# Performance work log

Measured on AMD Instinct MI355X. Metric: run time of the kernel, lower is better.

The kernel has to match this reference:

```python
import jax, jax.numpy as jnp
import numpy as np

I, H = 4, 64


def setup_inputs() -> dict:
    key = jax.random.key(0)
    ks = jax.random.split(key, 7)
    s_ih = 1.0 / np.sqrt(H)
    return {
        "x": jax.random.normal(ks[0], (8192, 512, I), dtype=jnp.float32),
        "W_ih": jax.random.uniform(ks[1], (4 * H, I), minval=-s_ih, maxval=s_ih, dtype=jnp.float32),
        "W_hh": jax.random.uniform(ks[2], (4 * H, H), minval=-s_ih, maxval=s_ih, dtype=jnp.float32),
        "b_ih": jax.random.uniform(ks[3], (4 * H,), minval=-s_ih, maxval=s_ih, dtype=jnp.float32),
        "b_hh": jax.random.uniform(ks[4], (4 * H,), minval=-s_ih, maxval=s_ih, dtype=jnp.float32),
        "W_fc": jax.random.uniform(ks[5], (1, H), minval=-s_ih, maxval=s_ih, dtype=jnp.float32),
        "b_fc": jax.random.uniform(ks[6], (1,), minval=-s_ih, maxval=s_ih, dtype=jnp.float32),
    }


def _lstm_last_hidden(x, W_ih, W_hh, b_ih, b_hh):
    # x: [B, T, I] batch_first; PyTorch gate order: i, f, g, o
    B = x.shape[0]
    # Precompute input projections for all timesteps in one GEMM: [T, B, 4H]
    xg = jnp.einsum('bti,gi->tbg', x, W_ih) + (b_ih + b_hh)

    def step(carry, xg_t):
        h, c = carry
        gates = xg_t + h @ W_hh.T  # [B, 4H]
        i, f, g, o = jnp.split(gates, 4, axis=-1)
        i = jax.nn.sigmoid(i)
        f = jax.nn.sigmoid(f)
        g = jnp.tanh(g)
        o = jax.nn.sigmoid(o)
        c = f * c + i * g
        h = o * jnp.tanh(c)
        return (h, c), None

    h0 = jnp.zeros((B, W_hh.shape[1]), dtype=x.dtype)
    c0 = jnp.zeros_like(h0)
    (h_n, _), _ = jax.lax.scan(step, (h0, c0), xg)
    return h_n  # [B, H]


def reference(x, W_ih, W_hh, b_ih, b_hh, W_fc, b_fc):
    h_n = _lstm_last_hidden(x, W_ih, W_hh, b_ih, b_hh)
    return h_n @ W_fc.T + b_fc  # [B, 1]
```

## Files before the change

### kernel.cpp

```cpp
#include <hip/hip_runtime.h>


typedef float f32x4 __attribute__((ext_vector_type(4)));
typedef _Float16 f16x8 __attribute__((ext_vector_type(8)));
typedef _Float16 f16x4 __attribute__((ext_vector_type(4)));

#define TSEQ 512
#define IDIM 4
#define BPB 16
#define TCH 32
#define L2E 1.44269504088896340736f

#if __has_builtin(__builtin_amdgcn_exp2f)
#define EX2(v) __builtin_amdgcn_exp2f(v)
#else
#define EX2(v) exp2f(v)
#endif
#define RCP(v) __builtin_amdgcn_rcpf(v)

__global__ __launch_bounds__(256, 2) void lstm_fused(
    const float* __restrict__ x,
    const float* __restrict__ W_ih,
    const float* __restrict__ W_hh,
    const float* __restrict__ b_ih,
    const float* __restrict__ b_hh,
    const float* __restrict__ W_fc,
    const float* __restrict__ b_fc,
    float* __restrict__ out)
{
    __shared__ __align__(16) _Float16 hbuf[2][BPB * 64];
    __shared__ __align__(8)  f16x4    xstage[BPB * 33];

    const int tid  = threadIdx.x;
    const int lane = tid & 63;
    const int wv   = tid >> 6;
    const int b0   = blockIdx.x * BPB;
    const int r    = lane & 15;
    const int g16  = lane >> 4;

    f16x8 bfrag[4][3];
    float bias[4];
    #pragma unroll
    for (int t4 = 0; t4 < 4; ++t4) {
        const float sc = (t4 == 2) ? 2.0f * L2E : L2E;
        const int g = t4 * 64 + wv * 16 + r;
        #pragma unroll
        for (int ks = 0; ks < 2; ++ks) {
            const float* p = W_hh + g * 64 + ks * 32 + g16 * 8;
            f16x8 f;
            #pragma unroll
            for (int j = 0; j < 8; ++j) f[j] = (_Float16)(p[j] * sc);
            bfrag[t4][ks] = f;
        }
        f16x8 f;
        #pragma unroll
        for (int j = 0; j < 8; ++j) f[j] = (_Float16)0.0f;
        if (g16 == 0) {
            #pragma unroll
            for (int j = 0; j < 4; ++j) f[j] = (_Float16)(W_ih[g * IDIM + j] * sc);
        }
        bfrag[t4][2] = f;
        bias[t4] = (b_ih[g] + b_hh[g]) * sc;
    }
    const float wfc = W_fc[lane];
    const float bfc = b_fc[0];

    float c_reg[4] = {0.f, 0.f, 0.f, 0.f};
    for (int i = tid; i < BPB * 64; i += 256) hbuf[0][i] = (_Float16)0.0f;

    const int bb0 = tid >> 5, tf = tid & 31;
    const float* xg0 = x + ((size_t)(b0 + bb0)     * TSEQ + tf) * IDIM;
    const float* xg1 = x + ((size_t)(b0 + bb0 + 8) * TSEQ + tf) * IDIM;
    float4 xn0 = *(const float4*)xg0;
    float4 xn1 = *(const float4*)xg1;

    const int hbase = r * 128;
    const int hs0 = ((g16 + 0) << 4) ^ ((r & 7) << 4);
    const int hs1 = ((g16 + 4) << 4) ^ ((r & 7) << 4);
    int hw[4];
    #pragma unroll
    for (int q = 0; q < 4; ++q) {
        const int bat = 4 * g16 + q;
        hw[q] = (bat * 128 + (wv * 16 + r) * 2) ^ ((bat & 7) << 4);
    }
    char* hb0 = (char*)&hbuf[0][0];
    char* hb1 = (char*)&hbuf[1][0];

    auto step = [&](int tt, const char* rb, char* wb) {
        f16x8 a0 = *(const f16x8*)(rb + hbase + hs0);
        f16x8 a1 = *(const f16x8*)(rb + hbase + hs1);
        f16x4 xv = f16x4{(_Float16)0.f, (_Float16)0.f, (_Float16)0.f, (_Float16)0.f};
        if (g16 == 0) xv = xstage[r * 33 + tt];
        f16x8 ax;
        ax[0] = xv[0]; ax[1] = xv[1]; ax[2] = xv[2]; ax[3] = xv[3];
        ax[4] = (_Float16)0.f; ax[5] = (_Float16)0.f;
        ax[6] = (_Float16)0.f; ax[7] = (_Float16)0.f;

        f32x4 acc[4];
        __builtin_amdgcn_s_setprio(1);
        #pragma unroll
        for (int t4 = 0; t4 < 4; ++t4) {
            f32x4 a; a[0] = a[1] = a[2] = a[3] = bias[t4];
            a = __builtin_amdgcn_mfma_f32_16x16x32_f16(a0, bfrag[t4][0], a, 0, 0, 0);
            a = __builtin_amdgcn_mfma_f32_16x16x32_f16(a1, bfrag[t4][1], a, 0, 0, 0);
            a = __builtin_amdgcn_mfma_f32_16x16x32_f16(ax, bfrag[t4][2], a, 0, 0, 0);
            acc[t4] = a;
        }
        __builtin_amdgcn_s_setprio(0);

        #pragma unroll
        for (int q = 0; q < 4; ++q) {
            float ei = EX2(-acc[0][q]);
            float ef = EX2(-acc[1][q]);
            float eg = EX2(-acc[2][q]);
            float eo = EX2(-acc[3][q]);
            float ig = (1.f - eg) * RCP((1.f + ei) * (1.f + eg));
            float ff = RCP(1.f + ef);
            float c  = ff * c_reg[q] + ig;
            c_reg[q] = c;
            float uc = fminf(fmaxf(c * (2.0f * L2E), -60.f), 60.f);
            float et = EX2(-uc);
            float h  = (1.f - et) * RCP((1.f + eo) * (1.f + et));
            *(_Float16*)(wb + hw[q]) = (_Float16)h;
        }
        __syncthreads();
    };

    for (int tc = 0; tc < TSEQ; tc += TCH) {
        f16x4 s0, s1;
        s0[0] = (_Float16)xn0.x; s0[1] = (_Float16)xn0.y;
        s0[2] = (_Float16)xn0.z; s0[3] = (_Float16)xn0.w;
        s1[0] = (_Float16)xn1.x; s1[1] = (_Float16)xn1.y;
        s1[2] = (_Float16)xn1.z; s1[3] = (_Float16)xn1.w;
        xstage[bb0 * 33 + tf]       = s0;
        xstage[(bb0 + 8) * 33 + tf] = s1;
        __syncthreads();
        if (tc + TCH < TSEQ) {
            xn0 = *(const float4*)(xg0 + (tc + TCH) * IDIM);
            xn1 = *(const float4*)(xg1 + (tc + TCH) * IDIM);
        }
        for (int tt = 0; tt < TCH; tt += 2) {
            step(tt,     hb0, hb1);
            step(tt + 1, hb1, hb0);
        }
    }

    #pragma unroll
    for (int q = 0; q < 4; ++q) {
        const int bat = 4 * wv + q;
        const int byte = (bat * 128 + lane * 2) ^ ((bat & 7) << 4);
        float hv = (float)*(const _Float16*)(hb0 + byte);
        float partial = hv * wfc;
        #pragma unroll
        for (int off = 32; off > 0; off >>= 1)
            partial += __shfl_down(partial, off);
        if (lane == 0) out[b0 + bat] = partial + bfc;
    }
}

extern "C" void kernel_launch(void* const* d_in, const int* in_sizes, int n_in,
                              void* d_out, int out_size, void* d_ws, size_t ws_size,
                              hipStream_t stream) {
    const float* x    = (const float*)d_in[0];
    const float* W_ih = (const float*)d_in[1];
    const float* W_hh = (const float*)d_in[2];
    const float* b_ih = (const float*)d_in[3];
    const float* b_hh = (const float*)d_in[4];
    const float* W_fc = (const float*)d_in[5];
    const float* b_fc = (const float*)d_in[6];
    float* out = (float*)d_out;

    const int B = in_sizes[0] / (TSEQ * IDIM);
    lstm_fused<<<B / BPB, 256, 0, stream>>>(x, W_ih, W_hh, b_ih, b_hh, W_fc, b_fc, out);
}
```

Measured before the change: 330.2 us.

## Halve batch per block and split gate nonlinearities across wave halves

Each block now handles 8 batch rows instead of 16, with launch bounds raised to 4 blocks per CU so more independent recurrences are resident. The MFMA tile is still 16 rows wide, so half of its rows are zero padding; lanes exchange accumulator halves via xor-32 shuffles so every lane computes transcendentals for only 2 useful rows instead of 4. The bias is folded into the x-projection MFMA as a hi/lo fp16 pair multiplied by constant ones, which frees the bias registers. The cost is half-wasted MFMA work, extra shuffles, and a small precision change in the bias.

```diff
diff --git a/kernel.cpp b/kernel.cpp
--- a/kernel.cpp
+++ b/kernel.cpp
@@ -7,7 +7,7 @@
 
 #define TSEQ 512
 #define IDIM 4
-#define BPB 16
+#define BPB 8
 #define TCH 32
 #define L2E 1.44269504088896340736f
 
@@ -18,7 +18,7 @@
 #endif
 #define RCP(v) __builtin_amdgcn_rcpf(v)
 
-__global__ __launch_bounds__(256, 2) void lstm_fused(
+__global__ __launch_bounds__(256, 4) void lstm_fused(
     const float* __restrict__ x,
     const float* __restrict__ W_ih,
     const float* __restrict__ W_hh,
@@ -28,8 +28,8 @@
     const float* __restrict__ b_fc,
     float* __restrict__ out)
 {
-    __shared__ __align__(16) _Float16 hbuf[2][BPB * 64];
-    __shared__ __align__(8)  f16x4    xstage[BPB * 33];
+    __shared__ __align__(16) _Float16 hbuf[2][16 * 64];
+    __shared__ __align__(8)  f16x4    xstage[16 * 33];
 
     const int tid  = threadIdx.x;
     const int lane = tid & 63;
@@ -39,7 +39,6 @@
     const int g16  = lane >> 4;
 
     f16x8 bfrag[4][3];
-    float bias[4];
     #pragma unroll
     for (int t4 = 0; t4 < 4; ++t4) {
         const float sc = (t4 == 2) ? 2.0f * L2E : L2E;
@@ -58,62 +57,78 @@
         if (g16 == 0) {
             #pragma unroll
             for (int j = 0; j < 4; ++j) f[j] = (_Float16)(W_ih[g * IDIM + j] * sc);
+            float biasf = (b_ih[g] + b_hh[g]) * sc;
+            _Float16 hi = (_Float16)biasf;
+            f[4] = hi;
+            f[5] = (_Float16)(biasf - (float)hi);
         }
         bfrag[t4][2] = f;
-        bias[t4] = (b_ih[g] + b_hh[g]) * sc;
     }
     const float wfc = W_fc[lane];
     const float bfc = b_fc[0];
+    const f32x4 zero4 = {0.f, 0.f, 0.f, 0.f};
 
-    float c_reg[4] = {0.f, 0.f, 0.f, 0.f};
-    for (int i = tid; i < BPB * 64; i += 256) hbuf[0][i] = (_Float16)0.0f;
+    float c_reg[2] = {0.f, 0.f};
+    for (int i = tid; i < 2 * 16 * 64; i += 256) ((_Float16*)hbuf)[i] = (_Float16)0.0f;
+    {
+        f16x4 z; z[0] = z[1] = z[2] = z[3] = (_Float16)0.0f;
+        for (int i = tid; i < 16 * 33; i += 256) xstage[i] = z;
+    }
 
-    const int bb0 = tid >> 5, tf = tid & 31;
-    const float* xg0 = x + ((size_t)(b0 + bb0)     * TSEQ + tf) * IDIM;
-    const float* xg1 = x + ((size_t)(b0 + bb0 + 8) * TSEQ + tf) * IDIM;
-    float4 xn0 = *(const float4*)xg0;
-    float4 xn1 = *(const float4*)xg1;
+    const int bb = tid >> 5, tf = tid & 31;
+    const float* xg = x + ((size_t)(b0 + bb) * TSEQ + tf) * IDIM;
+    float4 xn = *(const float4*)xg;
 
     const int hbase = r * 128;
     const int hs0 = ((g16 + 0) << 4) ^ ((r & 7) << 4);
     const int hs1 = ((g16 + 4) << 4) ^ ((r & 7) << 4);
-    int hw[4];
+    const int bat0 = ((g16 & 1) << 2) | ((g16 >> 1) << 1);
+    int hwb[2];
     #pragma unroll
-    for (int q = 0; q < 4; ++q) {
-        const int bat = 4 * g16 + q;
-        hw[q] = (bat * 128 + (wv * 16 + r) * 2) ^ ((bat & 7) << 4);
+    for (int q = 0; q < 2; ++q) {
+        const int bat = bat0 + q;
+        hwb[q] = (bat * 128 + (wv * 16 + r) * 2) ^ ((bat & 7) << 4);
     }
+    const bool lowhalf = (lane < 32);
     char* hb0 = (char*)&hbuf[0][0];
     char* hb1 = (char*)&hbuf[1][0];
 
     auto step = [&](int tt, const char* rb, char* wb) {
         f16x8 a0 = *(const f16x8*)(rb + hbase + hs0);
         f16x8 a1 = *(const f16x8*)(rb + hbase + hs1);
-        f16x4 xv = f16x4{(_Float16)0.f, (_Float16)0.f, (_Float16)0.f, (_Float16)0.f};
-        if (g16 == 0) xv = xstage[r * 33 + tt];
+        f16x4 xv = xstage[r * 33 + tt];
         f16x8 ax;
         ax[0] = xv[0]; ax[1] = xv[1]; ax[2] = xv[2]; ax[3] = xv[3];
-        ax[4] = (_Float16)0.f; ax[5] = (_Float16)0.f;
-        ax[6] = (_Float16)0.f; ax[7] = (_Float16)0.f;
+        ax[4] = (_Float16)1.0f; ax[5] = (_Float16)1.0f;
+        ax[6] = (_Float16)0.0f; ax[7] = (_Float16)0.0f;
 
         f32x4 acc[4];
         __builtin_amdgcn_s_setprio(1);
         #pragma unroll
         for (int t4 = 0; t4 < 4; ++t4) {
-            f32x4 a; a[0] = a[1] = a[2] = a[3] = bias[t4];
-            a = __builtin_amdgcn_mfma_f32_16x16x32_f16(a0, bfrag[t4][0], a, 0, 0, 0);
+            f32x4 a;
+            a = __builtin_amdgcn_mfma_f32_16x16x32_f16(a0, bfrag[t4][0], zero4, 0, 0, 0);
             a = __builtin_amdgcn_mfma_f32_16x16x32_f16(a1, bfrag[t4][1], a, 0, 0, 0);
             a = __builtin_amdgcn_mfma_f32_16x16x32_f16(ax, bfrag[t4][2], a, 0, 0, 0);
             acc[t4] = a;
         }
         __builtin_amdgcn_s_setprio(0);
 
+        float v[4][2];
         #pragma unroll
-        for (int q = 0; q < 4; ++q) {
-            float ei = EX2(-acc[0][q]);
-            float ef = EX2(-acc[1][q]);
-            float eg = EX2(-acc[2][q]);
-            float eo = EX2(-acc[3][q]);
+        for (int t4 = 0; t4 < 4; ++t4) {
+            float u2 = __shfl_xor(acc[t4][2], 32);
+            float u3 = __shfl_xor(acc[t4][3], 32);
+            v[t4][0] = lowhalf ? acc[t4][0] : u2;
+            v[t4][1] = lowhalf ? acc[t4][1] : u3;
+        }
+
+        #pragma unroll
+        for (int q = 0; q < 2; ++q) {
+            float ei = EX2(-v[0][q]);
+            float ef = EX2(-v[1][q]);
+            float eg = EX2(-v[2][q]);
+            float eo = EX2(-v[3][q]);
             float ig = (1.f - eg) * RCP((1.f + ei) * (1.f + eg));
             float ff = RCP(1.f + ef);
             float c  = ff * c_reg[q] + ig;
@@ -121,24 +136,20 @@
             float uc = fminf(fmaxf(c * (2.0f * L2E), -60.f), 60.f);
             float et = EX2(-uc);
             float h  = (1.f - et) * RCP((1.f + eo) * (1.f + et));
-            *(_Float16*)(wb + hw[q]) = (_Float16)h;
+            *(_Float16*)(wb + hwb[q]) = (_Float16)h;
         }
         __syncthreads();
     };
 
     for (int tc = 0; tc < TSEQ; tc += TCH) {
-        f16x4 s0, s1;
-        s0[0] = (_Float16)xn0.x; s0[1] = (_Float16)xn0.y;
-        s0[2] = (_Float16)xn0.z; s0[3] = (_Float16)xn0.w;
-        s1[0] = (_Float16)xn1.x; s1[1] = (_Float16)xn1.y;
-        s1[2] = (_Float16)xn1.z; s1[3] = (_Float16)xn1.w;
-        xstage[bb0 * 33 + tf]       = s0;
-        xstage[(bb0 + 8) * 33 + tf] = s1;
+        f16x4 s;
+        s[0] = (_Float16)xn.x; s[1] = (_Float16)xn.y;
+        s[2] = (_Float16)xn.z; s[3] = (_Float16)xn.w;
+        xstage[bb * 33 + tf] = s;
         __syncthreads();
-        if (tc + TCH < TSEQ) {
-            xn0 = *(const float4*)(xg0 + (tc + TCH) * IDIM);
-            xn1 = *(const float4*)(xg1 + (tc + TCH) * IDIM);
-        }
+        if (tc + TCH < TSEQ) xn = *(const float4*)(xg + (tc + TCH) * IDIM);
+
+        #pragma unroll 2
         for (int tt = 0; tt < TCH; tt += 2) {
             step(tt,     hb0, hb1);
             step(tt + 1, hb1, hb0);
@@ -146,8 +157,8 @@
     }
 
     #pragma unroll
-    for (int q = 0; q < 4; ++q) {
-        const int bat = 4 * wv + q;
+    for (int q = 0; q < 2; ++q) {
+        const int bat = wv * 2 + q;
         const int byte = (bat * 128 + lane * 2) ^ ((bat & 7) << 4);
         float hv = (float)*(const _Float16*)(hb0 + byte);
         float partial = hv * wfc;
```

New measurement: 450.2 us. 1.36x slower.

## Process two interleaved 16-row batch groups per block and fold bias into MFMA

Applied to the files above, without the earlier changes.

Each block now handles 32 batch rows as two independent 16-row groups, issuing both groups' MFMAs before either group's gate nonlinearities. This lets one group's matrix work overlap the other's transcendental math and halves the barriers per row. The bias moves into the input-projection MFMA as an fp16 hi/lo pair multiplied by constant ones, which frees the accumulator-initialisation registers. In exchange the grid is halved and launch bounds drop to one block per SIMD group, so occupancy falls and register pressure rises.

```diff
diff --git a/kernel.cpp b/kernel.cpp
--- a/kernel.cpp
+++ b/kernel.cpp
@@ -7,7 +7,7 @@
 
 #define TSEQ 512
 #define IDIM 4
-#define BPB 16
+#define BPB 32
 #define TCH 32
 #define L2E 1.44269504088896340736f
 
@@ -18,7 +18,7 @@
 #endif
 #define RCP(v) __builtin_amdgcn_rcpf(v)
 
-__global__ __launch_bounds__(256, 2) void lstm_fused(
+__global__ __launch_bounds__(256, 1) void lstm_fused(
     const float* __restrict__ x,
     const float* __restrict__ W_ih,
     const float* __restrict__ W_hh,
@@ -28,8 +28,8 @@
     const float* __restrict__ b_fc,
     float* __restrict__ out)
 {
-    __shared__ __align__(16) _Float16 hbuf[2][BPB * 64];
-    __shared__ __align__(8)  f16x4    xstage[BPB * 33];
+    __shared__ __align__(16) _Float16 hbuf[2][2][16 * 64];
+    __shared__ __align__(8)  f16x4    xstage[2][16][33];
 
     const int tid  = threadIdx.x;
     const int lane = tid & 63;
@@ -39,7 +39,6 @@
     const int g16  = lane >> 4;
 
     f16x8 bfrag[4][3];
-    float bias[4];
     #pragma unroll
     for (int t4 = 0; t4 < 4; ++t4) {
         const float sc = (t4 == 2) ? 2.0f * L2E : L2E;
@@ -58,21 +57,29 @@
         if (g16 == 0) {
             #pragma unroll
             for (int j = 0; j < 4; ++j) f[j] = (_Float16)(W_ih[g * IDIM + j] * sc);
+            float biasf = (b_ih[g] + b_hh[g]) * sc;
+            _Float16 hi = (_Float16)biasf;
+            f[4] = hi;
+            f[5] = (_Float16)(biasf - (float)hi);
         }
         bfrag[t4][2] = f;
-        bias[t4] = (b_ih[g] + b_hh[g]) * sc;
     }
     const float wfc = W_fc[lane];
     const float bfc = b_fc[0];
-
-    float c_reg[4] = {0.f, 0.f, 0.f, 0.f};
-    for (int i = tid; i < BPB * 64; i += 256) hbuf[0][i] = (_Float16)0.0f;
-
-    const int bb0 = tid >> 5, tf = tid & 31;
-    const float* xg0 = x + ((size_t)(b0 + bb0)     * TSEQ + tf) * IDIM;
-    const float* xg1 = x + ((size_t)(b0 + bb0 + 8) * TSEQ + tf) * IDIM;
-    float4 xn0 = *(const float4*)xg0;
-    float4 xn1 = *(const float4*)xg1;
+    const f32x4 zero4 = {0.f, 0.f, 0.f, 0.f};
+
+    float c0[4] = {0.f, 0.f, 0.f, 0.f};
+    float c1[4] = {0.f, 0.f, 0.f, 0.f};
+    for (int i = tid; i < 2 * 16 * 64; i += 256)
+        ((_Float16*)&hbuf[0][0][0])[i] = (_Float16)0.0f;
+
+    const int row  = tid >> 3;
+    const int grp  = row >> 4, lrow = row & 15;
+    const int st0  = (tid & 7) * 4;
+    const float* xg = x + ((size_t)(b0 + row) * TSEQ + st0) * IDIM;
+    float4 xp[4];
+    #pragma unroll
+    for (int j = 0; j < 4; ++j) xp[j] = *(const float4*)(xg + j * IDIM);
 
     const int hbase = r * 128;
     const int hs0 = ((g16 + 0) << 4) ^ ((r & 7) << 4);
@@ -83,31 +90,13 @@
         const int bat = 4 * g16 + q;
         hw[q] = (bat * 128 + (wv * 16 + r) * 2) ^ ((bat & 7) << 4);
     }
-    char* hb0 = (char*)&hbuf[0][0];
-    char* hb1 = (char*)&hbuf[1][0];
-
-    auto step = [&](int tt, const char* rb, char* wb) {
-        f16x8 a0 = *(const f16x8*)(rb + hbase + hs0);
-        f16x8 a1 = *(const f16x8*)(rb + hbase + hs1);
-        f16x4 xv = f16x4{(_Float16)0.f, (_Float16)0.f, (_Float16)0.f, (_Float16)0.f};
-        if (g16 == 0) xv = xstage[r * 33 + tt];
-        f16x8 ax;
-        ax[0] = xv[0]; ax[1] = xv[1]; ax[2] = xv[2]; ax[3] = xv[3];
-        ax[4] = (_Float16)0.f; ax[5] = (_Float16)0.f;
-        ax[6] = (_Float16)0.f; ax[7] = (_Float16)0.f;
-
-        f32x4 acc[4];
-        __builtin_amdgcn_s_setprio(1);
-        #pragma unroll
-        for (int t4 = 0; t4 < 4; ++t4) {
-            f32x4 a; a[0] = a[1] = a[2] = a[3] = bias[t4];
-            a = __builtin_amdgcn_mfma_f32_16x16x32_f16(a0, bfrag[t4][0], a, 0, 0, 0);
-            a = __builtin_amdgcn_mfma_f32_16x16x32_f16(a1, bfrag[t4][1], a, 0, 0, 0);
-            a = __builtin_amdgcn_mfma_f32_16x16x32_f16(ax, bfrag[t4][2], a, 0, 0, 0);
-            acc[t4] = a;
-        }
-        __builtin_amdgcn_s_setprio(0);
-
+    char* hb[2][2];
+    #pragma unroll
+    for (int p = 0; p < 2; ++p)
+        #pragma unroll
+        for (int g = 0; g < 2; ++g) hb[p][g] = (char*)&hbuf[p][g][0];
+
+    auto upd = [&](const f32x4* acc, float* cr, char* wb) {
         #pragma unroll
         for (int q = 0; q < 4; ++q) {
             float ei = EX2(-acc[0][q]);
@@ -116,45 +105,87 @@
             float eo = EX2(-acc[3][q]);
             float ig = (1.f - eg) * RCP((1.f + ei) * (1.f + eg));
             float ff = RCP(1.f + ef);
-            float c  = ff * c_reg[q] + ig;
-            c_reg[q] = c;
+            float c  = ff * cr[q] + ig;
+            cr[q] = c;
             float uc = fminf(fmaxf(c * (2.0f * L2E), -60.f), 60.f);
             float et = EX2(-uc);
             float h  = (1.f - et) * RCP((1.f + eo) * (1.f + et));
             *(_Float16*)(wb + hw[q]) = (_Float16)h;
         }
+    };
+
+    auto mfma12 = [&](f16x8 a0, f16x8 a1, f16x8 ax, f32x4* acc) {
+        __builtin_amdgcn_s_setprio(1);
+        #pragma unroll
+        for (int t4 = 0; t4 < 4; ++t4) {
+            f32x4 a;
+            a = __builtin_amdgcn_mfma_f32_16x16x32_f16(a0, bfrag[t4][0], zero4, 0, 0, 0);
+            a = __builtin_amdgcn_mfma_f32_16x16x32_f16(a1, bfrag[t4][1], a, 0, 0, 0);
+            a = __builtin_amdgcn_mfma_f32_16x16x32_f16(ax, bfrag[t4][2], a, 0, 0, 0);
+            acc[t4] = a;
+        }
+        __builtin_amdgcn_s_setprio(0);
+    };
+
+    auto step = [&](int tt, const char* rb0, const char* rb1, char* wb0, char* wb1) {
+        f16x8 a00 = *(const f16x8*)(rb0 + hbase + hs0);
+        f16x8 a01 = *(const f16x8*)(rb0 + hbase + hs1);
+        f16x4 xv0 = xstage[0][r][tt];
+        f16x8 ax0;
+        ax0[0] = xv0[0]; ax0[1] = xv0[1]; ax0[2] = xv0[2]; ax0[3] = xv0[3];
+        ax0[4] = (_Float16)1.0f; ax0[5] = (_Float16)1.0f;
+        ax0[6] = (_Float16)0.0f; ax0[7] = (_Float16)0.0f;
+        f32x4 acc0[4];
+        mfma12(a00, a01, ax0, acc0);
+
+        f16x8 a10 = *(const f16x8*)(rb1 + hbase + hs0);
+        f16x8 a11 = *(const f16x8*)(rb1 + hbase + hs1);
+        f16x4 xv1 = xstage[1][r][tt];
+        f16x8 ax1;
+        ax1[0] = xv1[0]; ax1[1] = xv1[1]; ax1[2] = xv1[2]; ax1[3] = xv1[3];
+        ax1[4] = (_Float16)1.0f; ax1[5] = (_Float16)1.0f;
+        ax1[6] = (_Float16)0.0f; ax1[7] = (_Float16)0.0f;
+        f32x4 acc1[4];
+        mfma12(a10, a11, ax1, acc1);
+
+        upd(acc0, c0, wb0);
+        upd(acc1, c1, wb1);
         __syncthreads();
     };
 
     for (int tc = 0; tc < TSEQ; tc += TCH) {
-        f16x4 s0, s1;
-        s0[0] = (_Float16)xn0.x; s0[1] = (_Float16)xn0.y;
-        s0[2] = (_Float16)xn0.z; s0[3] = (_Float16)xn0.w;
-        s1[0] = (_Float16)xn1.x; s1[1] = (_Float16)xn1.y;
-        s1[2] = (_Float16)xn1.z; s1[3] = (_Float16)xn1.w;
-        xstage[bb0 * 33 + tf]       = s0;
-        xstage[(bb0 + 8) * 33 + tf] = s1;
+        #pragma unroll
+        for (int j = 0; j < 4; ++j) {
+            f16x4 s;
+            s[0] = (_Float16)xp[j].x; s[1] = (_Float16)xp[j].y;
+            s[2] = (_Float16)xp[j].z; s[3] = (_Float16)xp[j].w;
+            xstage[grp][lrow][st0 + j] = s;
+        }
         __syncthreads();
         if (tc + TCH < TSEQ) {
-            xn0 = *(const float4*)(xg0 + (tc + TCH) * IDIM);
-            xn1 = *(const float4*)(xg1 + (tc + TCH) * IDIM);
+            #pragma unroll
+            for (int j = 0; j < 4; ++j)
+                xp[j] = *(const float4*)(xg + ((tc + TCH) + j) * IDIM);
         }
         for (int tt = 0; tt < TCH; tt += 2) {
-            step(tt,     hb0, hb1);
-            step(tt + 1, hb1, hb0);
-        }
-    }
-
-    #pragma unroll
-    for (int q = 0; q < 4; ++q) {
-        const int bat = 4 * wv + q;
-        const int byte = (bat * 128 + lane * 2) ^ ((bat & 7) << 4);
-        float hv = (float)*(const _Float16*)(hb0 + byte);
-        float partial = hv * wfc;
-        #pragma unroll
-        for (int off = 32; off > 0; off >>= 1)
-            partial += __shfl_down(partial, off);
-        if (lane == 0) out[b0 + bat] = partial + bfc;
+            step(tt,     hb[0][0], hb[0][1], hb[1][0], hb[1][1]);
+            step(tt + 1, hb[1][0], hb[1][1], hb[0][0], hb[0][1]);
+        }
+    }
+
+    #pragma unroll
+    for (int g = 0; g < 2; ++g) {
+        #pragma unroll
+        for (int q = 0; q < 4; ++q) {
+            const int bat = wv * 4 + q;
+            const int byte = (bat * 128 + lane * 2) ^ ((bat & 7) << 4);
+            float hv = (float)*(const _Float16*)(hb[0][g] + byte);
+            float partial = hv * wfc;
+            #pragma unroll
+            for (int off = 32; off > 0; off >>= 1)
+                partial += __shfl_down(partial, off);
+            if (lane == 0) out[b0 + g * 16 + bat] = partial + bfc;
+        }
     }
 }
 
```

New measurement: 412.1 us. 1.25x slower.

## Ping-pong two batch groups per block to overlap MFMA with gate transcendentals

Applied to the files above, without the earlier changes.

Each block now handles 32 sequences as two 16-row groups of four waves each. The groups alternate phases, so one group's MFMA gate matmul runs while the other group's sigmoid/tanh activation math runs, with a barrier between phases. This aims to hide the serial MFMA-then-transcendental latency of each recurrent step. It also folds the bias into the input MFMA using hi/lo fp16 bias columns, and simplifies the cell update to need one fewer reciprocal. The cost is twice as many barriers per timestep and larger 512-thread blocks, which may lower occupancy.

```diff
diff --git a/kernel.cpp b/kernel.cpp
--- a/kernel.cpp
+++ b/kernel.cpp
@@ -7,7 +7,7 @@
 
 #define TSEQ 512
 #define IDIM 4
-#define BPB 16
+#define BPB 32
 #define TCH 32
 #define L2E 1.44269504088896340736f
 
@@ -18,7 +18,7 @@
 #endif
 #define RCP(v) __builtin_amdgcn_rcpf(v)
 
-__global__ __launch_bounds__(256, 2) void lstm_fused(
+__global__ __launch_bounds__(512, 2) void lstm_fused(
     const float* __restrict__ x,
     const float* __restrict__ W_ih,
     const float* __restrict__ W_hh,
@@ -28,22 +28,23 @@
     const float* __restrict__ b_fc,
     float* __restrict__ out)
 {
-    __shared__ __align__(16) _Float16 hbuf[2][BPB * 64];
-    __shared__ __align__(8)  f16x4    xstage[BPB * 33];
+    __shared__ __align__(16) _Float16 hbuf[2][2][16 * 64];
+    __shared__ __align__(8)  f16x4    xstage[2][16][33];
 
     const int tid  = threadIdx.x;
     const int lane = tid & 63;
     const int wv   = tid >> 6;
+    const int grp  = wv >> 2;
+    const int wvl  = wv & 3;
     const int b0   = blockIdx.x * BPB;
     const int r    = lane & 15;
     const int g16  = lane >> 4;
 
     f16x8 bfrag[4][3];
-    float bias[4];
     #pragma unroll
     for (int t4 = 0; t4 < 4; ++t4) {
         const float sc = (t4 == 2) ? 2.0f * L2E : L2E;
-        const int g = t4 * 64 + wv * 16 + r;
+        const int g = t4 * 64 + wvl * 16 + r;
         #pragma unroll
         for (int ks = 0; ks < 2; ++ks) {
             const float* p = W_hh + g * 64 + ks * 32 + g16 * 8;
@@ -58,21 +59,27 @@
         if (g16 == 0) {
             #pragma unroll
             for (int j = 0; j < 4; ++j) f[j] = (_Float16)(W_ih[g * IDIM + j] * sc);
+            float biasf = (b_ih[g] + b_hh[g]) * sc;
+            _Float16 hi = (_Float16)biasf;
+            f[4] = hi;
+            f[5] = (_Float16)(biasf - (float)hi);
         }
         bfrag[t4][2] = f;
-        bias[t4] = (b_ih[g] + b_hh[g]) * sc;
     }
     const float wfc = W_fc[lane];
     const float bfc = b_fc[0];
+    const f32x4 zero4 = {0.f, 0.f, 0.f, 0.f};
 
     float c_reg[4] = {0.f, 0.f, 0.f, 0.f};
-    for (int i = tid; i < BPB * 64; i += 256) hbuf[0][i] = (_Float16)0.0f;
-
-    const int bb0 = tid >> 5, tf = tid & 31;
-    const float* xg0 = x + ((size_t)(b0 + bb0)     * TSEQ + tf) * IDIM;
-    const float* xg1 = x + ((size_t)(b0 + bb0 + 8) * TSEQ + tf) * IDIM;
-    float4 xn0 = *(const float4*)xg0;
-    float4 xn1 = *(const float4*)xg1;
+    for (int i = tid; i < 2 * 16 * 64; i += 512)
+        ((_Float16*)&hbuf[0][0][0])[i] = (_Float16)0.0f;
+
+    const int xrow = tid >> 4;
+    const int xgp  = xrow >> 4, xlr = xrow & 15;
+    const int xtf  = tid & 15;
+    const float* xg = x + ((size_t)(b0 + xrow) * TSEQ + 2 * xtf) * IDIM;
+    float4 xn0 = *(const float4*)xg;
+    float4 xn1 = *(const float4*)(xg + IDIM);
 
     const int hbase = r * 128;
     const int hs0 = ((g16 + 0) << 4) ^ ((r & 7) << 4);
@@ -81,80 +88,107 @@
     #pragma unroll
     for (int q = 0; q < 4; ++q) {
         const int bat = 4 * g16 + q;
-        hw[q] = (bat * 128 + (wv * 16 + r) * 2) ^ ((bat & 7) << 4);
-    }
-    char* hb0 = (char*)&hbuf[0][0];
-    char* hb1 = (char*)&hbuf[1][0];
-
-    auto step = [&](int tt, const char* rb, char* wb) {
+        hw[q] = (bat * 128 + (wvl * 16 + r) * 2) ^ ((bat & 7) << 4);
+    }
+    char* hbB = (char*)&hbuf[0][0][0];
+    const int gofs = grp * 2048;
+    const f16x4* xsb = &xstage[grp][r][0];
+
+    auto STAGE = [&]() {
+        f16x4 s0, s1;
+        s0[0] = (_Float16)xn0.x; s0[1] = (_Float16)xn0.y;
+        s0[2] = (_Float16)xn0.z; s0[3] = (_Float16)xn0.w;
+        s1[0] = (_Float16)xn1.x; s1[1] = (_Float16)xn1.y;
+        s1[2] = (_Float16)xn1.z; s1[3] = (_Float16)xn1.w;
+        xstage[xgp][xlr][2 * xtf]     = s0;
+        xstage[xgp][xlr][2 * xtf + 1] = s1;
+    };
+
+    auto MFMA = [&](int parity, int tt, f32x4* acc) {
+        const char* rb = hbB + parity * 4096 + gofs;
         f16x8 a0 = *(const f16x8*)(rb + hbase + hs0);
         f16x8 a1 = *(const f16x8*)(rb + hbase + hs1);
-        f16x4 xv = f16x4{(_Float16)0.f, (_Float16)0.f, (_Float16)0.f, (_Float16)0.f};
-        if (g16 == 0) xv = xstage[r * 33 + tt];
+        f16x4 xv = xsb[tt];
         f16x8 ax;
         ax[0] = xv[0]; ax[1] = xv[1]; ax[2] = xv[2]; ax[3] = xv[3];
-        ax[4] = (_Float16)0.f; ax[5] = (_Float16)0.f;
-        ax[6] = (_Float16)0.f; ax[7] = (_Float16)0.f;
-
-        f32x4 acc[4];
+        ax[4] = (_Float16)1.0f; ax[5] = (_Float16)1.0f;
+        ax[6] = (_Float16)0.0f; ax[7] = (_Float16)0.0f;
         __builtin_amdgcn_s_setprio(1);
         #pragma unroll
         for (int t4 = 0; t4 < 4; ++t4) {
-            f32x4 a; a[0] = a[1] = a[2] = a[3] = bias[t4];
-            a = __builtin_amdgcn_mfma_f32_16x16x32_f16(a0, bfrag[t4][0], a, 0, 0, 0);
+            f32x4 a;
+            a = __builtin_amdgcn_mfma_f32_16x16x32_f16(a0, bfrag[t4][0], zero4, 0, 0, 0);
             a = __builtin_amdgcn_mfma_f32_16x16x32_f16(a1, bfrag[t4][1], a, 0, 0, 0);
             a = __builtin_amdgcn_mfma_f32_16x16x32_f16(ax, bfrag[t4][2], a, 0, 0, 0);
             acc[t4] = a;
         }
         __builtin_amdgcn_s_setprio(0);
-
+    };
+
+    auto TRANS = [&](int parityW, const f32x4* acc) {
+        char* wb = hbB + parityW * 4096 + gofs;
         #pragma unroll
         for (int q = 0; q < 4; ++q) {
             float ei = EX2(-acc[0][q]);
             float ef = EX2(-acc[1][q]);
             float eg = EX2(-acc[2][q]);
             float eo = EX2(-acc[3][q]);
-            float ig = (1.f - eg) * RCP((1.f + ei) * (1.f + eg));
-            float ff = RCP(1.f + ef);
-            float c  = ff * c_reg[q] + ig;
+            float A  = 1.f + ei, F = 1.f + ef;
+            float Gp = 1.f + eg, Gm = 1.f - eg;
+            float P   = A * Gp;
+            float num = c_reg[q] * P + Gm * F;
+            float c   = num * RCP(P * F);
             c_reg[q] = c;
             float uc = fminf(fmaxf(c * (2.0f * L2E), -60.f), 60.f);
             float et = EX2(-uc);
             float h  = (1.f - et) * RCP((1.f + eo) * (1.f + et));
             *(_Float16*)(wb + hw[q]) = (_Float16)h;
         }
+    };
+
+    STAGE();
+    __syncthreads();
+    xn0 = *(const float4*)(xg + TCH * IDIM);
+    xn1 = *(const float4*)(xg + TCH * IDIM + IDIM);
+
+    f32x4 acc[4];
+    if (grp == 0) MFMA(0, 0, acc);
+    __syncthreads();
+    if (grp == 0) TRANS(1, acc);
+    else          MFMA(0, 0, acc);
+    __syncthreads();
+
+    for (int t = 1; t < TSEQ; ++t) {
+        if ((t & (TCH - 1)) == 0) {
+            STAGE();
+            __syncthreads();
+            if (t + TCH < TSEQ) {
+                xn0 = *(const float4*)(xg + (size_t)(t + TCH) * IDIM);
+                xn1 = *(const float4*)(xg + (size_t)(t + TCH) * IDIM + IDIM);
+            }
+        }
+        const int tt = t & (TCH - 1);
+        const int p  = t & 1;
+        if (grp == 0) MFMA(p, tt, acc);
+        else          TRANS(p, acc);
         __syncthreads();
-    };
-
-    for (int tc = 0; tc < TSEQ; tc += TCH) {
-        f16x4 s0, s1;
-        s0[0] = (_Float16)xn0.x; s0[1] = (_Float16)xn0.y;
-        s0[2] = (_Float16)xn0.z; s0[3] = (_Float16)xn0.w;
-        s1[0] = (_Float16)xn1.x; s1[1] = (_Float16)xn1.y;
-        s1[2] = (_Float16)xn1.z; s1[3] = (_Float16)xn1.w;
-        xstage[bb0 * 33 + tf]       = s0;
-        xstage[(bb0 + 8) * 33 + tf] = s1;
+        if (grp == 0) TRANS(p ^ 1, acc);
+        else          MFMA(p, tt, acc);
         __syncthreads();
-        if (tc + TCH < TSEQ) {
-            xn0 = *(const float4*)(xg0 + (tc + TCH) * IDIM);
-            xn1 = *(const float4*)(xg1 + (tc + TCH) * IDIM);
-        }
-        for (int tt = 0; tt < TCH; tt += 2) {
-            step(tt,     hb0, hb1);
-            step(tt + 1, hb1, hb0);
-        }
-    }
+    }
+    if (grp == 1) TRANS(0, acc);
+    __syncthreads();
 
     #pragma unroll
     for (int q = 0; q < 4; ++q) {
-        const int bat = 4 * wv + q;
+        const int bat  = wvl * 4 + q;
         const int byte = (bat * 128 + lane * 2) ^ ((bat & 7) << 4);
-        float hv = (float)*(const _Float16*)(hb0 + byte);
+        float hv = (float)*(const _Float16*)(hbB + gofs + byte);
         float partial = hv * wfc;
         #pragma unroll
         for (int off = 32; off > 0; off >>= 1)
             partial += __shfl_down(partial, off);
-        if (lane == 0) out[b0 + bat] = partial + bfc;
+        if (lane == 0) out[b0 + grp * 16 + bat] = partial + bfc;
     }
 }
 
@@ -171,5 +205,5 @@
     float* out = (float*)d_out;
 
     const int B = in_sizes[0] / (TSEQ * IDIM);
-    lstm_fused<<<B / BPB, 256, 0, stream>>>(x, W_ih, W_hh, b_ih, b_hh, W_fc, b_fc, out);
+    lstm_fused<<<B / BPB, 512, 0, stream>>>(x, W_ih, W_hh, b_ih, b_hh, W_fc, b_fc, out);
 }
```

Measured after the change: 422.2 us. +27.8%, slower.
